# Performance work log

Hardware: AMD Instinct MI355X
Metric: run time of the kernel (lower is better)

## Reference

```python
import jax, jax.numpy as jnp
import numpy as np
import math

V, D, H, L, MLP = 32000, 1024, 16, 4, 4
B, T = 2, 1024
HD = D // H
ALIBI_BIAS_MAX = 8.0
EPS = 1e-5


def _ln(x, g, b):
    m = jnp.mean(x, -1, keepdims=True)
    v = jnp.mean((x - m) ** 2, -1, keepdims=True)
    return (x - m) * jax.lax.rsqrt(v + EPS) * g + b


def setup_inputs() -> dict:
    key = jax.random.key(0)
    ks = jax.random.split(key, 12)
    s = 0.02
    inp = {
        "input_ids": jax.random.randint(ks[0], (B, T), 0, V),
        "wte": jax.random.normal(ks[1], (V, D), jnp.float32) * s,
        "ln1_g": jnp.ones((L, D), jnp.float32),
        "ln1_b": jnp.zeros((L, D), jnp.float32),
        "attn_w": jax.random.normal(ks[2], (L, 3 * D, D), jnp.float32) * s,
        "attn_b": jnp.zeros((L, 3 * D), jnp.float32),
        "proj_w": jax.random.normal(ks[3], (L, D, D), jnp.float32) * s,
        "proj_b": jnp.zeros((L, D), jnp.float32),
        "ln2_g": jnp.ones((L, D), jnp.float32),
        "ln2_b": jnp.zeros((L, D), jnp.float32),
        "fc_w": jax.random.normal(ks[4], (L, MLP * D, D), jnp.float32) * s,
        "fc_b": jnp.zeros((L, MLP * D), jnp.float32),
        "fc2_w": jax.random.normal(ks[5], (L, D, MLP * D), jnp.float32) * s,
        "fc2_b": jnp.zeros((L, D), jnp.float32),
        "lnf_g": jnp.ones((D,), jnp.float32),
        "lnf_b": jnp.zeros((D,), jnp.float32),
        "lm_head_w": jax.random.normal(ks[6], (V, D), jnp.float32) * s,
    }
    return inp


def reference(input_ids, wte, ln1_g, ln1_b, attn_w, attn_b, proj_w, proj_b,
              ln2_g, ln2_b, fc_w, fc_b, fc2_w, fc2_b, lnf_g, lnf_b, lm_head_w):
    b, t = input_ids.shape
    x = wte[input_ids]  # [B,T,D]

    # causal + ALiBi bias, [H,T,T]
    pos = jnp.arange(t)
    rel = -jnp.abs(pos[None, :] - pos[:, None]).astype(jnp.float32)  # -|i-j|
    m = jnp.arange(1, H + 1, dtype=jnp.float32) * (ALIBI_BIAS_MAX / H)
    alibi = rel[None, :, :] * (2.0 ** (-m))[:, None, None]
    causal = jnp.where(pos[None, :] > pos[:, None], -jnp.inf, 0.0)
    bias = alibi + causal[None]
    scale = 1.0 / math.sqrt(HD)

    def block(x, p):
        l1g, l1b, aw, ab, pw, pb, l2g, l2b, fw, fb, f2w, f2b = p
        h = _ln(x, l1g, l1b)
        qkv = h @ aw.T + ab  # [B,T,3D]
        q, k, v = jnp.split(qkv, 3, axis=-1)
        q = q.reshape(b, t, H, HD).transpose(0, 2, 1, 3)
        k = k.reshape(b, t, H, HD).transpose(0, 2, 1, 3)
        v = v.reshape(b, t, H, HD).transpose(0, 2, 1, 3)
        att = jnp.einsum('bhid,bhjd->bhij', q, k) * scale + bias[None]
        att = jax.nn.softmax(att, axis=-1)
        y = jnp.einsum('bhij,bhjd->bhid', att, v)
        y = y.transpose(0, 2, 1, 3).reshape(b, t, D)
        x = x + (y @ pw.T + pb)
        h2 = _ln(x, l2g, l2b)
        x = x + (jax.nn.gelu(h2 @ fw.T + fb, approximate=False) @ f2w.T + f2b)
        return x, None

    x, _ = jax.lax.scan(
        block, x,
        (ln1_g, ln1_b, attn_w, attn_b, proj_w, proj_b,
         ln2_g, ln2_b, fc_w, fc_b, fc2_w, fc2_b))
    x = _ln(x, lnf_g, lnf_b)
    logits = x @ lm_head_w.T  # [B,T,V]
    return logits
```

## Files before the change

### kernel.cpp

```cpp
#include <hip/hip_runtime.h>
#include <hip/hip_bf16.h>
#include <math.h>

typedef __hip_bfloat16 bf16;
typedef __attribute__((ext_vector_type(4))) float f32x4;
typedef __attribute__((ext_vector_type(8))) short short8;

constexpr int Bc = 2, Tc = 1024, Dc = 1024, Hc = 16, Lc = 4, MLPc = 4096, Vc = 32000, HDc = 64;

__device__ __forceinline__ unsigned short f2bu(float f) {
    __hip_bfloat16 h = __float2bfloat16(f);
    unsigned short u;
    __builtin_memcpy(&u, &h, 2);
    return u;
}

__device__ __forceinline__ void gl2lds16(const bf16* g, bf16* l) {
    __builtin_amdgcn_global_load_lds(
        (const __attribute__((address_space(1))) void*)g,
        (__attribute__((address_space(3))) void*)l, 16, 0, 0);
}

enum { EPI_BIAS_BF16 = 0, EPI_GELU = 1, EPI_RESADD = 2, EPI_F32 = 3 };

template <int EPI>
__device__ __forceinline__ void epi_store(float v, int row, int col, void* Cv,
                                          int ldc, const float* bias) {
    if constexpr (EPI == EPI_BIAS_BF16) {
        v += bias[col];
        ((bf16*)Cv)[(size_t)row * ldc + col] = __float2bfloat16(v);
    } else if constexpr (EPI == EPI_GELU) {
        v += bias[col];
        v = 0.5f * v * (1.0f + erff(v * 0.70710678118f));
        ((bf16*)Cv)[(size_t)row * ldc + col] = __float2bfloat16(v);
    } else if constexpr (EPI == EPI_RESADD) {
        float* C = (float*)Cv;
        size_t idx = (size_t)row * ldc + col;
        C[idx] += v + bias[col];
    } else if constexpr (EPI == EPI_F32) {
        ((float*)Cv)[(size_t)row * ldc + col] = v;
    }
}

template <int BM, int BN, int BK, int EPI, bool SWZG>
__global__ __launch_bounds__(256) void gemm_fast(
    const bf16* __restrict__ A, int lda,
    const bf16* __restrict__ Bm, int ldb,
    void* __restrict__ Cv, int ldc,
    const float* __restrict__ bias, int K)
{
    static_assert(BK == 64, "staging geometry assumes BK=64");
    __shared__ alignas(16) bf16 As[2][BM][BK];
    __shared__ alignas(16) bf16 Bs[2][BN][BK];

    const int tid = threadIdx.x;
    const int lane = tid & 63;
    const int w = tid >> 6;
    const int wm = w >> 1, wn = w & 1;
    constexpr int WM = BM / 2, WN = BN / 2;
    constexpr int FM = WM / 16, FN = WN / 16;
    constexpr int RPI = 512 / BK;
    constexpr int AI = BM / (4 * RPI);
    constexpr int BI = BN / (4 * RPI);

    int im, in;
    if constexpr (SWZG) {
        int nwg = gridDim.x * gridDim.y;
        int orig = blockIdx.y * gridDim.x + blockIdx.x;
        int q = nwg >> 3, rr = nwg & 7, xcd = orig & 7, lid = orig >> 3;
        int wg = (xcd < rr ? xcd * (q + 1) : rr * (q + 1) + (xcd - rr) * q) + lid;
        im = wg % gridDim.x;
        in = wg / gridDim.x;
    } else {
        im = blockIdx.y;
        in = blockIdx.x;
    }

    const bf16* Ab = A + (size_t)im * BM * lda;
    const bf16* Bb = Bm + (size_t)in * BN * ldb;

    const int sr = lane >> 3;
    const int scs = (((lane & 7) ^ sr) * 8);
    const int lr = lane & 15, lq = lane >> 4;

    f32x4 acc[FM][FN];
#pragma unroll
    for (int i = 0; i < FM; i++)
#pragma unroll
        for (int j = 0; j < FN; j++) acc[i][j] = (f32x4){0.f, 0.f, 0.f, 0.f};

    auto stage = [&](int buf, int k0) {
#pragma unroll
        for (int i = 0; i < AI; i++) {
            int row = (w * AI + i) * RPI;
            gl2lds16(Ab + (size_t)(row + sr) * lda + k0 + scs, &As[buf][row][0]);
        }
#pragma unroll
        for (int i = 0; i < BI; i++) {
            int row = (w * BI + i) * RPI;
            gl2lds16(Bb + (size_t)(row + sr) * ldb + k0 + scs, &Bs[buf][row][0]);
        }
    };

    const int NT = K / BK;
    stage(0, 0);
    __syncthreads();

    for (int t = 0; t < NT; t++) {
        const int cur = t & 1;
        if (t + 1 < NT) stage(cur ^ 1, (t + 1) * BK);

        const char* Abase = (const char*)&As[cur][0][0];
        const char* Bbase = (const char*)&Bs[cur][0][0];
#pragma unroll
        for (int kk = 0; kk < BK / 32; kk++) {
            short8 af[FM], bfr[FN];
#pragma unroll
            for (int i = 0; i < FM; i++) {
                int r = wm * WM + i * 16 + lr;
                int cb = (kk * 64 + lq * 16) ^ ((r & 7) << 4);
                af[i] = *reinterpret_cast<const short8*>(Abase + (size_t)r * (BK * 2) + cb);
            }
#pragma unroll
            for (int j = 0; j < FN; j++) {
                int r = wn * WN + j * 16 + lr;
                int cb = (kk * 64 + lq * 16) ^ ((r & 7) << 4);
                bfr[j] = *reinterpret_cast<const short8*>(Bbase + (size_t)r * (BK * 2) + cb);
            }
#pragma unroll
            for (int i = 0; i < FM; i++)
#pragma unroll
                for (int j = 0; j < FN; j++)
                    acc[i][j] = __builtin_amdgcn_mfma_f32_16x16x32_bf16(af[i], bfr[j], acc[i][j], 0, 0, 0);
        }
        __syncthreads();
    }

#pragma unroll
    for (int i = 0; i < FM; i++)
#pragma unroll
        for (int j = 0; j < FN; j++)
#pragma unroll
            for (int r = 0; r < 4; r++) {
                int row = im * BM + wm * WM + i * 16 + lq * 4 + r;
                int col = in * BN + wn * WN + j * 16 + lr;
                epi_store<EPI>(acc[i][j][r], row, col, Cv, ldc, bias);
            }
}

template <int BM, int BN, int BK, int EPI>
__global__ __launch_bounds__(256) void gemm_bt_f32(
    const bf16* __restrict__ A, int lda,
    const float* __restrict__ Bm, int ldb,
    void* __restrict__ Cv, int ldc,
    const float* __restrict__ bias, int K)
{
    constexpr int BKP = BK + 8;
    __shared__ bf16 As[BM][BKP];
    __shared__ bf16 Bs[BN][BKP];
    const int tid = threadIdx.x;
    const int lane = tid & 63;
    const int w = tid >> 6;
    const int wm = w >> 1, wn = w & 1;
    constexpr int WM = BM / 2, WN = BN / 2;
    constexpr int FM = WM / 16, FN = WN / 16;
    const int bx = blockIdx.x, by = blockIdx.y;
    const bf16* Ab = A + (size_t)by * BM * lda;
    const float* Bb = Bm + (size_t)bx * BN * ldb;
    f32x4 acc[FM][FN];
#pragma unroll
    for (int i = 0; i < FM; i++)
#pragma unroll
        for (int j = 0; j < FN; j++) acc[i][j] = (f32x4){0.f, 0.f, 0.f, 0.f};
    const int lr = lane & 15, lq = lane >> 4;
    for (int k0 = 0; k0 < K; k0 += BK) {
        constexpr int AC = (BM * BK) / (256 * 8);
#pragma unroll
        for (int i = 0; i < AC; i++) {
            int c = tid + i * 256;
            int row = c / (BK / 8);
            int kc = (c % (BK / 8)) * 8;
            *reinterpret_cast<int4*>(&As[row][kc]) =
                *reinterpret_cast<const int4*>(Ab + (size_t)row * lda + k0 + kc);
        }
        constexpr int BC = (BN * BK) / (256 * 4);
#pragma unroll
        for (int i = 0; i < BC; i++) {
            int c = tid + i * 256;
            int row = c / (BK / 4);
            int kc = (c % (BK / 4)) * 4;
            float4 v = *reinterpret_cast<const float4*>(Bb + (size_t)row * ldb + k0 + kc);
            unsigned long long p = (unsigned long long)f2bu(v.x) |
                                   ((unsigned long long)f2bu(v.y) << 16) |
                                   ((unsigned long long)f2bu(v.z) << 32) |
                                   ((unsigned long long)f2bu(v.w) << 48);
            *reinterpret_cast<unsigned long long*>(&Bs[row][kc]) = p;
        }
        __syncthreads();
#pragma unroll
        for (int kk = 0; kk < BK / 32; kk++) {
            short8 af[FM], bfr[FN];
#pragma unroll
            for (int i = 0; i < FM; i++)
                af[i] = *reinterpret_cast<const short8*>(&As[wm * WM + i * 16 + lr][kk * 32 + lq * 8]);
#pragma unroll
            for (int j = 0; j < FN; j++)
                bfr[j] = *reinterpret_cast<const short8*>(&Bs[wn * WN + j * 16 + lr][kk * 32 + lq * 8]);
#pragma unroll
            for (int i = 0; i < FM; i++)
#pragma unroll
                for (int j = 0; j < FN; j++)
                    acc[i][j] = __builtin_amdgcn_mfma_f32_16x16x32_bf16(af[i], bfr[j], acc[i][j], 0, 0, 0);
        }
        __syncthreads();
    }
#pragma unroll
    for (int i = 0; i < FM; i++)
#pragma unroll
        for (int j = 0; j < FN; j++)
#pragma unroll
            for (int r = 0; r < 4; r++) {
                int row = by * BM + wm * WM + i * 16 + lq * 4 + r;
                int col = bx * BN + wn * WN + j * 16 + lr;
                epi_store<EPI>(acc[i][j][r], row, col, Cv, ldc, bias);
            }
}

__global__ __launch_bounds__(256) void flash_attn(
    const bf16* __restrict__ q, const bf16* __restrict__ kbuf,
    const bf16* __restrict__ vt, bf16* __restrict__ y)
{
    __shared__ alignas(16) bf16 Ks[128 * 64];
    __shared__ alignas(16) bf16 Vs[64 * 128];
    __shared__ alignas(16) bf16 Ps[4 * 16 * 136];

    const int tid = threadIdx.x;
    const int lane = tid & 63;
    const int w = tid >> 6;
    const int lr = lane & 15, lq = lane >> 4;
    const int qi = (int)gridDim.x - 1 - (int)blockIdx.x;
    const int z = blockIdx.y;
    const int b = z >> 4, h = z & 15;
    const float slope = exp2f(-0.5f * (float)(h + 1));

    const bf16* qz = q + (size_t)z * (Tc * HDc);
    const bf16* kz = kbuf + (size_t)z * (Tc * HDc);
    const bf16* vz = vt + (size_t)z * (HDc * Tc);

    const int rowbase = qi * 64 + w * 16;

    short8 qf[2];
#pragma unroll
    for (int kk = 0; kk < 2; kk++)
        qf[kk] = *reinterpret_cast<const short8*>(
            qz + (size_t)(rowbase + lr) * HDc + kk * 32 + lq * 8);

    float m_old[4], l_sum[4];
#pragma unroll
    for (int r = 0; r < 4; r++) { m_old[r] = -3.0e38f; l_sum[r] = 0.f; }
    f32x4 o[4];
#pragma unroll
    for (int dj = 0; dj < 4; dj++) o[dj] = (f32x4){0.f, 0.f, 0.f, 0.f};

    bf16* Pw = Ps + w * 16 * 136;

    const int nkv = (qi * 64 + 63) / 128 + 1;
    for (int kv = 0; kv < nkv; kv++) {
#pragma unroll
        for (int i = 0; i < 4; i++) {
            int rbase = w * 32 + i * 8;
            int row = rbase + (lane >> 3);
            int slot = lane & 7;
            gl2lds16(kz + (size_t)(kv * 128 + row) * HDc + ((slot ^ (row & 7)) * 8),
                     &Ks[rbase * 64]);
        }
#pragma unroll
        for (int i = 0; i < 4; i++) {
            int rbase = w * 16 + i * 4;
            int row = rbase + lq;
            gl2lds16(vz + (size_t)row * Tc + kv * 128 + ((lr ^ (row & 7)) * 8),
                     &Vs[rbase * 128]);
        }
        __syncthreads();

        f32x4 s[8];
#pragma unroll
        for (int j = 0; j < 8; j++) s[j] = (f32x4){0.f, 0.f, 0.f, 0.f};
#pragma unroll
        for (int kk = 0; kk < 2; kk++) {
#pragma unroll
            for (int j = 0; j < 8; j++) {
                int row = j * 16 + lr;
                int cb = ((kk * 4 + lq) ^ (row & 7)) << 4;
                short8 bfr = *reinterpret_cast<const short8*>(
                    (const char*)Ks + row * 128 + cb);
                s[j] = __builtin_amdgcn_mfma_f32_16x16x32_bf16(qf[kk], bfr, s[j], 0, 0, 0);
            }
        }

        float mt[4];
#pragma unroll
        for (int r = 0; r < 4; r++) mt[r] = -3.0e38f;
#pragma unroll
        for (int j = 0; j < 8; j++) {
            int col = kv * 128 + j * 16 + lr;
#pragma unroll
            for (int r = 0; r < 4; r++) {
                int rowg = rowbase + lq * 4 + r;
                float v = s[j][r] * 0.125f - (float)(rowg - col) * slope;
                v = (col > rowg) ? -3.0e38f : v;
                s[j][r] = v;
                mt[r] = fmaxf(mt[r], v);
            }
        }
#pragma unroll
        for (int r = 0; r < 4; r++)
#pragma unroll
            for (int off = 1; off < 16; off <<= 1)
                mt[r] = fmaxf(mt[r], __shfl_xor(mt[r], off));

        float f[4], rs[4];
#pragma unroll
        for (int r = 0; r < 4; r++) {
            float mn = fmaxf(m_old[r], mt[r]);
            f[r] = __expf(m_old[r] - mn);
            m_old[r] = mn;
            rs[r] = 0.f;
        }
#pragma unroll
        for (int j = 0; j < 8; j++)
#pragma unroll
            for (int r = 0; r < 4; r++) {
                float p = __expf(s[j][r] - m_old[r]);
                s[j][r] = p;
                rs[r] += p;
            }
#pragma unroll
        for (int r = 0; r < 4; r++) {
#pragma unroll
            for (int off = 1; off < 16; off <<= 1)
                rs[r] += __shfl_xor(rs[r], off);
            l_sum[r] = l_sum[r] * f[r] + rs[r];
        }

#pragma unroll
        for (int j = 0; j < 8; j++)
#pragma unroll
            for (int r = 0; r < 4; r++)
                Pw[(lq * 4 + r) * 136 + j * 16 + lr] = __float2bfloat16(s[j][r]);

#pragma unroll
        for (int dj = 0; dj < 4; dj++)
#pragma unroll
            for (int r = 0; r < 4; r++) o[dj][r] *= f[r];

        __syncthreads();

#pragma unroll
        for (int kk = 0; kk < 4; kk++) {
            short8 pa = *reinterpret_cast<const short8*>(
                (const char*)Pw + lr * 272 + kk * 64 + lq * 16);
#pragma unroll
            for (int dj = 0; dj < 4; dj++) {
                int row = dj * 16 + lr;
                int cb = ((kk * 4 + lq) ^ (row & 7)) << 4;
                short8 vb = *reinterpret_cast<const short8*>(
                    (const char*)Vs + row * 256 + cb);
                o[dj] = __builtin_amdgcn_mfma_f32_16x16x32_bf16(pa, vb, o[dj], 0, 0, 0);
            }
        }
        __syncthreads();
    }

#pragma unroll
    for (int dj = 0; dj < 4; dj++)
#pragma unroll
        for (int r = 0; r < 4; r++) {
            int rowg = rowbase + lq * 4 + r;
            float outv = o[dj][r] / l_sum[r];
            y[((size_t)b * Tc + rowg) * Dc + h * HDc + dj * 16 + lr] =
                __float2bfloat16(outv);
        }
}

__global__ __launch_bounds__(256) void f2b8(const float* __restrict__ in,
                                            bf16* __restrict__ out, long n) {
    long i = ((long)blockIdx.x * 256 + threadIdx.x) * 8;
    if (i >= n) return;
    float4 a = *reinterpret_cast<const float4*>(in + i);
    float4 b = *reinterpret_cast<const float4*>(in + i + 4);
    unsigned long long p0 = (unsigned long long)f2bu(a.x) |
                            ((unsigned long long)f2bu(a.y) << 16) |
                            ((unsigned long long)f2bu(a.z) << 32) |
                            ((unsigned long long)f2bu(a.w) << 48);
    unsigned long long p1 = (unsigned long long)f2bu(b.x) |
                            ((unsigned long long)f2bu(b.y) << 16) |
                            ((unsigned long long)f2bu(b.z) << 32) |
                            ((unsigned long long)f2bu(b.w) << 48);
    *reinterpret_cast<unsigned long long*>(out + i) = p0;
    *reinterpret_cast<unsigned long long*>(out + i + 4) = p1;
}

__global__ __launch_bounds__(256) void embed_kernel(const int* __restrict__ ids,
                                                    const float* __restrict__ wte,
                                                    float* __restrict__ x) {
    int row = blockIdx.x;
    int t = threadIdx.x;
    int id = ids[row];
    reinterpret_cast<float4*>(x + (size_t)row * Dc)[t] =
        reinterpret_cast<const float4*>(wte + (size_t)id * Dc)[t];
}

__global__ __launch_bounds__(256) void ln_kernel(const float* __restrict__ x,
                                                 const float* __restrict__ g,
                                                 const float* __restrict__ b,
                                                 bf16* __restrict__ out) {
    int row = blockIdx.x;
    int t = threadIdx.x;
    const float4 v = reinterpret_cast<const float4*>(x + (size_t)row * Dc)[t];
    float s = v.x + v.y + v.z + v.w;
    float s2 = v.x * v.x + v.y * v.y + v.z * v.z + v.w * v.w;
#pragma unroll
    for (int o = 32; o > 0; o >>= 1) {
        s += __shfl_down(s, o);
        s2 += __shfl_down(s2, o);
    }
    __shared__ float sm[8];
    int wid = t >> 6, ln = t & 63;
    if (ln == 0) { sm[wid] = s; sm[4 + wid] = s2; }
    __syncthreads();
    if (t == 0) {
        float ts = sm[0] + sm[1] + sm[2] + sm[3];
        float ts2 = sm[4] + sm[5] + sm[6] + sm[7];
        sm[0] = ts; sm[4] = ts2;
    }
    __syncthreads();
    float mean = sm[0] * (1.0f / Dc);
    float var = sm[4] * (1.0f / Dc) - mean * mean;
    float rstd = rsqrtf(var + 1e-5f);
    int c0 = t * 4;
    float vv[4] = {v.x, v.y, v.z, v.w};
    unsigned long long p = 0;
#pragma unroll
    for (int j = 0; j < 4; j++) {
        float val = (vv[j] - mean) * rstd * g[c0 + j] + b[c0 + j];
        p |= (unsigned long long)f2bu(val) << (16 * j);
    }
    *reinterpret_cast<unsigned long long*>(out + (size_t)row * Dc + c0) = p;
}

__global__ __launch_bounds__(256) void unpack_qkv(const bf16* __restrict__ qkv,
                                                  bf16* __restrict__ q,
                                                  bf16* __restrict__ k,
                                                  bf16* __restrict__ vt) {
    int idx = blockIdx.x * 256 + threadIdx.x;
    {
        int bt = idx >> 7;
        int c = idx & 127;
        int b = bt >> 10, t = bt & (Tc - 1);
        int h = c >> 3;
        int hd = (c & 7) * 8;
        size_t dst = (((size_t)(b * Hc + h) * Tc + t) * HDc + hd) / 8;
        const int4* src = reinterpret_cast<const int4*>(qkv + (size_t)bt * 3 * Dc);
        reinterpret_cast<int4*>(q)[dst] = src[c];
        reinterpret_cast<int4*>(k)[dst] = src[128 + c];
    }
    {
        int t0 = (idx & 127) * 8;
        int rest = idx >> 7;
        int hd = rest & 63;
        int z = rest >> 6;
        int b = z >> 4, h = z & 15;
        const bf16* src = qkv + ((size_t)b * Tc) * 3 * Dc + 2 * Dc + h * HDc + hd;
        unsigned long long p0 = 0, p1 = 0;
#pragma unroll
        for (int i = 0; i < 4; i++) {
            unsigned short u;
            __builtin_memcpy(&u, src + (size_t)(t0 + i) * 3 * Dc, 2);
            p0 |= (unsigned long long)u << (16 * i);
        }
#pragma unroll
        for (int i = 0; i < 4; i++) {
            unsigned short u;
            __builtin_memcpy(&u, src + (size_t)(t0 + 4 + i) * 3 * Dc, 2);
            p1 |= (unsigned long long)u << (16 * i);
        }
        bf16* dst = vt + ((size_t)z * HDc + hd) * Tc + t0;
        *reinterpret_cast<unsigned long long*>(dst) = p0;
        *reinterpret_cast<unsigned long long*>(dst + 4) = p1;
    }
}

extern "C" void kernel_launch(void* const* d_in, const int* in_sizes, int n_in,
                              void* d_out, int out_size, void* d_ws, size_t ws_size,
                              hipStream_t stream) {
    const int* ids = (const int*)d_in[0];
    const float* wte = (const float*)d_in[1];
    const float* ln1g = (const float*)d_in[2];
    const float* ln1b = (const float*)d_in[3];
    const float* attw = (const float*)d_in[4];
    const float* attb = (const float*)d_in[5];
    const float* projw = (const float*)d_in[6];
    const float* projb = (const float*)d_in[7];
    const float* ln2g = (const float*)d_in[8];
    const float* ln2b = (const float*)d_in[9];
    const float* fcw = (const float*)d_in[10];
    const float* fcb = (const float*)d_in[11];
    const float* fc2w = (const float*)d_in[12];
    const float* fc2b = (const float*)d_in[13];
    const float* lnfg = (const float*)d_in[14];
    const float* lnfb = (const float*)d_in[15];
    const float* lmw = (const float*)d_in[16];

    const int M = Bc * Tc;
    char* ws = (char*)d_ws;
    size_t off = 0;
    auto carve = [&](size_t bytes) { char* p = ws + off; off += (bytes + 255) & ~(size_t)255; return p; };

    float* x = (float*)carve((size_t)M * Dc * 4);
    bf16* h = (bf16*)carve((size_t)M * Dc * 2);
    bf16* qkv = (bf16*)carve((size_t)M * 3 * Dc * 2);
    bf16* q = (bf16*)carve((size_t)Bc * Hc * Tc * HDc * 2);
    bf16* kb = (bf16*)carve((size_t)Bc * Hc * Tc * HDc * 2);
    bf16* vt = (bf16*)carve((size_t)Bc * Hc * Tc * HDc * 2);
    bf16* y = (bf16*)carve((size_t)M * Dc * 2);
    bf16* mlp = (bf16*)carve((size_t)M * MLPc * 2);

    const long nLM = (long)Vc * Dc;
    bool has_wlm = ws_size >= off + (size_t)nLM * 2;
    bf16* wlm = nullptr;
    if (has_wlm) wlm = (bf16*)carve((size_t)nLM * 2);

    const long nAW = (long)Lc * 3 * Dc * Dc;
    const long nPW = (long)Lc * Dc * Dc;
    const long nFW = (long)Lc * MLPc * Dc;
    const long nF2W = (long)Lc * Dc * MLPc;
    bf16* awAll = (bf16*)d_out;
    bf16* pwAll = awAll + nAW;
    bf16* fwAll = pwAll + nPW;
    bf16* f2wAll = fwAll + nFW;

    embed_kernel<<<M, 256, 0, stream>>>(ids, wte, x);

    f2b8<<<(int)(nAW / 8 / 256), 256, 0, stream>>>(attw, awAll, nAW);
    f2b8<<<(int)(nPW / 8 / 256), 256, 0, stream>>>(projw, pwAll, nPW);
    f2b8<<<(int)(nFW / 8 / 256), 256, 0, stream>>>(fcw, fwAll, nFW);
    f2b8<<<(int)(nF2W / 8 / 256), 256, 0, stream>>>(fc2w, f2wAll, nF2W);
    if (has_wlm)
        f2b8<<<(int)(nLM / 8 / 256), 256, 0, stream>>>(lmw, wlm, nLM);

    for (int l = 0; l < Lc; l++) {
        bf16* aw_b = awAll + (size_t)l * 3 * Dc * Dc;
        bf16* pw_b = pwAll + (size_t)l * Dc * Dc;
        bf16* fw_b = fwAll + (size_t)l * MLPc * Dc;
        bf16* f2w_b = f2wAll + (size_t)l * Dc * MLPc;

        ln_kernel<<<M, 256, 0, stream>>>(x, ln1g + l * Dc, ln1b + l * Dc, h);

        gemm_fast<128, 128, 64, EPI_BIAS_BF16, true>
            <<<dim3(M / 128, 3 * Dc / 128, 1), 256, 0, stream>>>(
                h, Dc, aw_b, Dc, qkv, 3 * Dc, attb + l * 3 * Dc, Dc);

        unpack_qkv<<<(M * Dc / 8) / 256, 256, 0, stream>>>(qkv, q, kb, vt);

        flash_attn<<<dim3(Tc / 64, Bc * Hc), 256, 0, stream>>>(q, kb, vt, y);

        gemm_fast<128, 128, 64, EPI_RESADD, true>
            <<<dim3(M / 128, Dc / 128, 1), 256, 0, stream>>>(
                y, Dc, pw_b, Dc, x, Dc, projb + l * Dc, Dc);

        ln_kernel<<<M, 256, 0, stream>>>(x, ln2g + l * Dc, ln2b + l * Dc, h);

        gemm_fast<128, 128, 64, EPI_GELU, true>
            <<<dim3(M / 128, MLPc / 128, 1), 256, 0, stream>>>(
                h, Dc, fw_b, Dc, mlp, MLPc, fcb + l * MLPc, Dc);

        gemm_fast<128, 128, 64, EPI_RESADD, true>
            <<<dim3(M / 128, Dc / 128, 1), 256, 0, stream>>>(
                mlp, MLPc, f2w_b, MLPc, x, Dc, fc2b + l * Dc, MLPc);
    }

    ln_kernel<<<M, 256, 0, stream>>>(x, lnfg, lnfb, h);

    if (has_wlm)
        gemm_fast<128, 128, 64, EPI_F32, true>
            <<<dim3(M / 128, Vc / 128, 1), 256, 0, stream>>>(
                h, Dc, wlm, Dc, (float*)d_out, Vc, nullptr, Dc);
    else
        gemm_bt_f32<128, 128, 64, EPI_F32>
            <<<dim3(Vc / 128, M / 128, 1), 256, 0, stream>>>(
                h, Dc, lmw, Dc, (float*)d_out, Vc, nullptr, Dc);
}
```

Measured before the change: 1.309 ms.

## Add 256x256 eight-wave GEMM with phased prefetch for LM head

Introduces a new GEMM kernel using 256x256 tiles, 512 threads (8 waves), double-buffered LDS filled by direct global-to-LDS loads split into four phases interleaved with MFMA compute, plus XCD-aware workgroup remapping. It is used only for the final LM-head projection (M=2048, N=32000) in place of the 128x128 kernel. The goal is more data reuse per tile and better overlap of loads with matrix math on the largest GEMM. Risks include higher register pressure, only 8x125 workgroups, and a fragile hand-tuned vmcnt/barrier schedule.

```diff
diff --git a/kernel.cpp b/kernel.cpp
--- a/kernel.cpp
+++ b/kernel.cpp
@@ -40,6 +40,127 @@
     } else if constexpr (EPI == EPI_F32) {
         ((float*)Cv)[(size_t)row * ldc + col] = v;
     }
+}
+
+template <int EPI>
+__global__ __launch_bounds__(512) void gemm_8p(
+    const bf16* __restrict__ A, int lda,
+    const bf16* __restrict__ Bm, int ldb,
+    void* __restrict__ Cv, int ldc,
+    const float* __restrict__ bias, int K)
+{
+    constexpr int BM = 256, BN = 256, BK = 64;
+    __shared__ alignas(16) bf16 As[2][BM][BK];
+    __shared__ alignas(16) bf16 Bs[2][BN][BK];
+
+    const int tid = threadIdx.x;
+    const int lane = tid & 63;
+    const int w = tid >> 6;
+    const int wm = w >> 2;
+    const int wn = w & 3;
+
+    int nwg = gridDim.x * gridDim.y;
+    int orig = blockIdx.y * gridDim.x + blockIdx.x;
+    int q = nwg >> 3, rr = nwg & 7, xcd = orig & 7, lid = orig >> 3;
+    int wg = (xcd < rr ? xcd * (q + 1) : rr * (q + 1) + (xcd - rr) * q) + lid;
+    int im = wg % gridDim.x;
+    int in = wg / gridDim.x;
+
+    const bf16* Ab = A + (size_t)im * BM * lda;
+    const bf16* Bb = Bm + (size_t)in * BN * ldb;
+
+    const int sr = lane >> 3;
+    const int scs = ((lane & 7) ^ sr) * 8;
+    const int lr = lane & 15, lq = lane >> 4;
+
+    f32x4 acc[2][2][4][2];
+#pragma unroll
+    for (int a = 0; a < 2; a++)
+#pragma unroll
+        for (int b = 0; b < 2; b++)
+#pragma unroll
+            for (int c = 0; c < 4; c++)
+#pragma unroll
+                for (int d = 0; d < 2; d++) acc[a][b][c][d] = (f32x4){0.f, 0.f, 0.f, 0.f};
+
+    const int NT = K / BK;
+
+    auto stage_half = [&](int buf, int hf, int k0) {
+        const bf16* gp = (hf & 1) ? Bb : Ab;
+        const int ld = (hf & 1) ? ldb : lda;
+        bf16* ls = (hf & 1) ? &Bs[buf][0][0] : &As[buf][0][0];
+        const int half = hf >> 1;
+#pragma unroll
+        for (int i = 0; i < 2; i++) {
+            int r0 = half * 128 + i * 64 + w * 8;
+            gl2lds16(gp + (size_t)(r0 + sr) * ld + k0 + scs, ls + r0 * BK);
+        }
+    };
+
+#pragma unroll
+    for (int hf = 0; hf < 4; hf++) stage_half(0, hf, 0);
+    asm volatile("s_waitcnt vmcnt(0)" ::: "memory");
+    __builtin_amdgcn_s_barrier();
+    asm volatile("" ::: "memory");
+
+    for (int t = 0; t < NT; t++) {
+        const int cur = t & 1;
+        const char* Abase = (const char*)&As[cur][0][0];
+        const char* Bbase = (const char*)&Bs[cur][0][0];
+#pragma unroll
+        for (int ph = 0; ph < 4; ph++) {
+            const int mh = ph & 1, nh = ph >> 1;
+            short8 af[4][2], bfv[2][2];
+#pragma unroll
+            for (int fi = 0; fi < 4; fi++) {
+                int r = mh * 128 + wm * 64 + fi * 16 + lr;
+#pragma unroll
+                for (int kk = 0; kk < 2; kk++) {
+                    int cb = (kk * 64 + lq * 16) ^ ((r & 7) << 4);
+                    af[fi][kk] = *reinterpret_cast<const short8*>(Abase + (size_t)r * 128 + cb);
+                }
+            }
+#pragma unroll
+            for (int fj = 0; fj < 2; fj++) {
+                int r = nh * 128 + wn * 32 + fj * 16 + lr;
+#pragma unroll
+                for (int kk = 0; kk < 2; kk++) {
+                    int cb = (kk * 64 + lq * 16) ^ ((r & 7) << 4);
+                    bfv[fj][kk] = *reinterpret_cast<const short8*>(Bbase + (size_t)r * 128 + cb);
+                }
+            }
+            if (t + 1 < NT) stage_half(cur ^ 1, ph, (t + 1) * BK);
+            __builtin_amdgcn_s_barrier();
+            __builtin_amdgcn_s_setprio(1);
+#pragma unroll
+            for (int kk = 0; kk < 2; kk++)
+#pragma unroll
+                for (int fi = 0; fi < 4; fi++)
+#pragma unroll
+                    for (int fj = 0; fj < 2; fj++)
+                        acc[mh][nh][fi][fj] = __builtin_amdgcn_mfma_f32_16x16x32_bf16(
+                            af[fi][kk], bfv[fj][kk], acc[mh][nh][fi][fj], 0, 0, 0);
+            __builtin_amdgcn_s_setprio(0);
+            if (ph != 2) asm volatile("s_waitcnt vmcnt(4)" ::: "memory");
+            __builtin_amdgcn_s_barrier();
+            asm volatile("" ::: "memory");
+        }
+    }
+
+#pragma unroll
+    for (int mh = 0; mh < 2; mh++)
+#pragma unroll
+        for (int nh = 0; nh < 2; nh++)
+#pragma unroll
+            for (int fi = 0; fi < 4; fi++)
+#pragma unroll
+                for (int fj = 0; fj < 2; fj++)
+#pragma unroll
+                    for (int r = 0; r < 4; r++) {
+                        int row = im * 256 + mh * 128 + wm * 64 + fi * 16 + lq * 4 + r;
+                        int col = in * 256 + nh * 128 + wn * 32 + fj * 16 + lr;
+                        epi_store<EPI>(acc[mh][nh][fi][fj][r], row, col, Cv, ldc, bias);
+                    }
 }
 
 template <int BM, int BN, int BK, int EPI, bool SWZG>
@@ -583,8 +704,8 @@
     ln_kernel<<<M, 256, 0, stream>>>(x, lnfg, lnfb, h);
 
     if (has_wlm)
-        gemm_fast<128, 128, 64, EPI_F32, true>
-            <<<dim3(M / 128, Vc / 128, 1), 256, 0, stream>>>(
+        gemm_8p<EPI_F32>
+            <<<dim3(M / 256, Vc / 256, 1), 512, 0, stream>>>(
                 h, Dc, wlm, Dc, (float*)d_out, Vc, nullptr, Dc);
     else
         gemm_bt_f32<128, 128, 64, EPI_F32>
```

Measured after the change: 1.298 ms. Within noise of the previous version (-0.9%).
